# Performance work log

Hardware: AMD Instinct MI355X
Metric: run time of the kernel (lower is better)

The kernel has to match this reference:

```python
import jax, jax.numpy as jnp
import numpy as np

DIM = 4096
N_HEADS = 32
HEAD_DIM = 128
N_KV_HEADS = 8
KV_REPEATS = N_HEADS // N_KV_HEADS
SLIDING_WINDOW = 4096
SEQLEN = 2048
SCALE = HEAD_DIM ** -0.5
NEG = -1e9


def calculate_rope(x, cos, sin):
    # x: [S, H, D]; cos/sin: [S, D//2] applied to interleaved channel pairs
    x1, x2 = x[..., ::2], x[..., 1::2]
    c, s = cos[:, None, :], sin[:, None, :]
    r1 = x1 * c - x2 * s
    r2 = x1 * s + x2 * c
    return jnp.stack([r1, r2], axis=-1).reshape(x.shape)


def setup_inputs() -> dict:
    key = jax.random.key(0)
    ks = jax.random.split(key, 8)
    x = jax.random.normal(ks[0], (SEQLEN, DIM), dtype=jnp.float32)
    # rotary tables
    inv_freq = 1.0 / (10000.0 ** (np.arange(0, HEAD_DIM, 2, dtype=np.float32) / HEAD_DIM))
    t = np.arange(SEQLEN, dtype=np.float32)
    freqs = np.outer(t, inv_freq)  # [S, D/2]
    cos_freq = jnp.asarray(np.cos(freqs), dtype=jnp.float32)
    sin_freq = jnp.asarray(np.sin(freqs), dtype=jnp.float32)
    positions = jnp.arange(SEQLEN, dtype=jnp.int32)
    # causal sliding-window additive mask
    i = np.arange(SEQLEN)[:, None]
    j = np.arange(SEQLEN)[None, :]
    allow = (j <= i) & (j > i - SLIDING_WINDOW)
    mask = jnp.asarray(np.where(allow, 0.0, NEG), dtype=jnp.float32)
    cache_k = jnp.zeros((SLIDING_WINDOW, N_KV_HEADS, HEAD_DIM), dtype=jnp.float32)
    cache_v = jnp.zeros((SLIDING_WINDOW, N_KV_HEADS, HEAD_DIM), dtype=jnp.float32)
    # eqx.nn.Linear weights have shape (out_features, in_features)
    sd = DIM ** -0.5
    wq = jax.random.normal(ks[1], (N_HEADS * HEAD_DIM, DIM), dtype=jnp.float32) * sd
    wk = jax.random.normal(ks[2], (N_KV_HEADS * HEAD_DIM, DIM), dtype=jnp.float32) * sd
    wv = jax.random.normal(ks[3], (N_KV_HEADS * HEAD_DIM, DIM), dtype=jnp.float32) * sd
    wo = jax.random.normal(ks[4], (DIM, N_HEADS * HEAD_DIM), dtype=jnp.float32) * (N_HEADS * HEAD_DIM) ** -0.5
    return {"x": x, "cos_freq": cos_freq, "sin_freq": sin_freq, "positions": positions,
            "mask": mask, "cache_k": cache_k, "cache_v": cache_v,
            "wq": wq, "wk": wk, "wv": wv, "wo": wo}


def reference(x, cos_freq, sin_freq, positions, mask, cache_k, cache_v, wq, wk, wv, wo):
    seqlen = x.shape[0]
    xq = (x @ wq.T).reshape(seqlen, N_HEADS, HEAD_DIM)
    xk = (x @ wk.T).reshape(seqlen, N_KV_HEADS, HEAD_DIM)
    xv = (x @ wv.T).reshape(seqlen, N_KV_HEADS, HEAD_DIM)
    xq = calculate_rope(xq, cos_freq, sin_freq)
    xk = calculate_rope(xk, cos_freq, sin_freq)
    # prefill branch (positions.shape[0] > 1): scatter into sliding-window cache
    cache_k = cache_k.at[positions, :, :].set(xk[positions, :, :], mode='drop')
    cache_v = cache_v.at[positions, :, :].set(xv[positions, :, :], mode='drop')
    # GQA repeat kv heads
    k = jnp.repeat(xk, KV_REPEATS, axis=1)  # [S, H, D]
    v = jnp.repeat(xv, KV_REPEATS, axis=1)
    # scores: [H, Sq, Sk]
    scores = jnp.einsum('qhd,khd->hqk', xq, k) * SCALE
    scores = scores + mask[None, ...]
    probs = jax.nn.softmax(scores.astype(jnp.float32), axis=-1).astype(xq.dtype)
    out = jnp.einsum('hqk,khd->qhd', probs, v).reshape(seqlen, N_HEADS * HEAD_DIM)
    output = out @ wo.T
    return output, cache_k, cache_v
```

## Files before the change

### kernel.cpp

```cpp
#include <hip/hip_runtime.h>

typedef unsigned short ushort_t;
typedef unsigned int uint_t;
typedef __attribute__((ext_vector_type(8))) short bf16x8;
typedef __attribute__((ext_vector_type(4))) float floatx4;
typedef __attribute__((ext_vector_type(16))) float floatx16;

#define SEQ 2048
#define DIM 4096
#define NH 32
#define NKV 8
#define HD 128
#define KVDIM 1024
#define QKVN 6144

__device__ __forceinline__ ushort_t f2b(float f) {
  union { float f; uint_t u; } x; x.f = f;
  uint_t u = x.u;
  u += 0x7fffu + ((u >> 16) & 1u);
  return (ushort_t)(u >> 16);
}

#define GLOAD_LDS(g, l) \
  __builtin_amdgcn_global_load_lds((const __attribute__((address_space(1))) void*)(g), \
                                   (__attribute__((address_space(3))) void*)(l), 16, 0, 0)

#define BARX() asm volatile("s_barrier" ::: "memory")
#define WAIT_VM(n) asm volatile("s_waitcnt vmcnt(" #n ")" ::: "memory")

__global__ __launch_bounds__(256) void cvt_all(const float* __restrict__ x,
                                               const float* __restrict__ wq,
                                               const float* __restrict__ wk,
                                               const float* __restrict__ wv,
                                               const float* __restrict__ wo,
                                               ushort_t* __restrict__ xb,
                                               ushort_t* __restrict__ wqkvb,
                                               ushort_t* __restrict__ wob) {
  int b = blockIdx.x;
  const float* src; ushort_t* dst; int i;
  if (b < 4096)       { src = x;  dst = xb;               i = b * 256 + threadIdx.x; }
  else if (b < 12288) { src = wq; dst = wqkvb;            i = (b - 4096) * 256 + threadIdx.x; }
  else if (b < 14336) { src = wk; dst = wqkvb + 16777216; i = (b - 12288) * 256 + threadIdx.x; }
  else if (b < 16384) { src = wv; dst = wqkvb + 20971520; i = (b - 14336) * 256 + threadIdx.x; }
  else                { src = wo; dst = wob;              i = (b - 16384) * 256 + threadIdx.x; }
  const float4* s = (const float4*)src;
  float4 a = s[2 * i], c = s[2 * i + 1];
  union { ushort_t u[8]; uint4 v; } o;
  o.u[0] = f2b(a.x); o.u[1] = f2b(a.y); o.u[2] = f2b(a.z); o.u[3] = f2b(a.w);
  o.u[4] = f2b(c.x); o.u[5] = f2b(c.y); o.u[6] = f2b(c.z); o.u[7] = f2b(c.w);
  ((uint4*)dst)[i] = o.v;
}

__global__ __launch_bounds__(512, 2) void gemm8p(const ushort_t* __restrict__ A,
                                                 const ushort_t* __restrict__ B,
                                                 float* __restrict__ C,
                                                 int N, int K) {
  __shared__ __attribute__((aligned(16))) ushort_t sA[2][8192];
  __shared__ __attribute__((aligned(16))) ushort_t sB[2][16384];

  int tid = threadIdx.x;
  int lane = tid & 63;
  int w = tid >> 6;
  int wm = w >> 2, wn = w & 3;
  int l15 = lane & 15, l4 = lane >> 4;
  int e7 = l15 & 7;
  int co0 = ((l4 ^ e7) << 3);
  int co1 = co0 ^ 32;

  int nwg = (int)gridDim.x;
  int ntn = N >> 8;
  int lin = ((int)blockIdx.x & 7) * (nwg >> 3) + ((int)blockIdx.x >> 3);
  int m0 = (lin / ntn) << 7;
  int n0 = (lin % ntn) << 8;

  int nkt = K >> 6;
  int niter = nkt >> 1;

  int r0 = tid >> 3;
  int c0 = ((tid & 7) ^ (r0 & 7)) << 3;
  const ushort_t* sa0 = A + (size_t)(m0 + r0) * K + c0;
  const ushort_t* sb0 = B + (size_t)(n0 + r0) * K + c0;
  const ushort_t* sb1 = sb0 + (size_t)128 * K;
  int d0 = (tid & ~63) << 3;
  size_t ek = (size_t)64 * K;

#define STA(kk, s)  do { GLOAD_LDS(sa0 + (kk), &sA[s][d0]); \
                         GLOAD_LDS(sa0 + ek + (kk), &sA[s][d0 + 4096]); } while (0)
#define STB0(kk, s) do { GLOAD_LDS(sb0 + (kk), &sB[s][d0]); \
                         GLOAD_LDS(sb0 + ek + (kk), &sB[s][d0 + 4096]); } while (0)
#define STB1(kk, s) do { GLOAD_LDS(sb1 + (kk), &sB[s][8192 + d0]); \
                         GLOAD_LDS(sb1 + ek + (kk), &sB[s][8192 + d0 + 4096]); } while (0)

  floatx4 acc[4][4] = {};
  bf16x8 a[4][2], b[4][2];

#define RDA2(s, RG) do { const ushort_t* pa = &sA[s][(wm * 64 + l15) * 64]; \
  _Pragma("unroll") for (int rg = 0; rg < 2; ++rg) { \
    a[RG + rg][0] = *(const bf16x8*)&pa[(RG + rg) * 1024 + co0]; \
    a[RG + rg][1] = *(const bf16x8*)&pa[(RG + rg) * 1024 + co1]; } } while (0)
#define RDB2(s, CG) do { const ushort_t* pb = &sB[s][(wn * 64 + l15) * 64]; \
  _Pragma("unroll") for (int cg = 0; cg < 2; ++cg) { \
    b[CG + cg][0] = *(const bf16x8*)&pb[(CG + cg) * 1024 + co0]; \
    b[CG + cg][1] = *(const bf16x8*)&pb[(CG + cg) * 1024 + co1]; } } while (0)

#define QUAD(RG, CG) do { __builtin_amdgcn_s_setprio(1); \
  _Pragma("unroll") for (int rg = 0; rg < 2; ++rg) \
  _Pragma("unroll") for (int cg = 0; cg < 2; ++cg) \
  _Pragma("unroll") for (int ks = 0; ks < 2; ++ks) \
    acc[RG + rg][CG + cg] = __builtin_amdgcn_mfma_f32_16x16x32_bf16( \
        a[RG + rg][ks], b[CG + cg][ks], acc[RG + rg][CG + cg], 0, 0, 0); \
  __builtin_amdgcn_s_setprio(0); } while (0)

  STA(0, 0); STB0(0, 0); STB1(0, 0);
  STA(64, 1); STB0(64, 1);
  WAIT_VM(4);
  BARX();

#pragma unroll 1
  for (int i = 0; i < niter; ++i) {
    int k1 = (2 * i + 1) << 6;
    int t2 = 2 * i + 2; if (t2 > nkt - 1) t2 = nkt - 1;
    int t3 = 2 * i + 3; if (t3 > nkt - 1) t3 = nkt - 1;
    int k2 = t2 << 6, k3 = t3 << 6;

    RDA2(0, 0); RDB2(0, 0); RDA2(0, 2);
    STB1(k1, 1);
    BARX(); QUAD(0, 0); BARX();
    RDB2(0, 2);
    STA(k2, 0);
    BARX(); QUAD(0, 2); BARX();
    STB0(k2, 0);
    BARX(); QUAD(2, 0); BARX();
    STB1(k2, 0);
    WAIT_VM(6);
    BARX(); QUAD(2, 2); BARX();

    RDA2(1, 0); RDB2(1, 0); RDA2(1, 2);
    BARX(); QUAD(0, 0); BARX();
    RDB2(1, 2);
    STA(k3, 1);
    BARX(); QUAD(0, 2); BARX();
    STB0(k3, 1);
    BARX(); QUAD(2, 0); BARX();
    WAIT_VM(4);
    BARX(); QUAD(2, 2); BARX();
  }

#pragma unroll
  for (int rg = 0; rg < 4; ++rg)
#pragma unroll
    for (int cg = 0; cg < 4; ++cg) {
      float* cp = C + (size_t)(m0 + wm * 64 + rg * 16 + l4 * 4) * N
                    + (n0 + wn * 64 + cg * 16 + l15);
#pragma unroll
      for (int r = 0; r < 4; ++r) cp[(size_t)r * N] = acc[rg][cg][r];
    }
#undef STA
#undef STB0
#undef STB1
#undef RDA2
#undef RDB2
#undef QUAD
}

__global__ __launch_bounds__(256) void posteps(const float* __restrict__ qkv,
                                               const float* __restrict__ cosf,
                                               const float* __restrict__ sinf,
                                               ushort_t* __restrict__ qb,
                                               ushort_t* __restrict__ kb,
                                               float* __restrict__ out) {
  int b = blockIdx.x;
  if (b < 16384) {
    const float QS = 1.4426950408889634f * 0.08838834764831845f;
    int idx = b * 256 + threadIdx.x;
    int pos = idx >> 11;
    int p = idx & 2047;
    int h = p >> 6, i = p & 63;
    size_t sb = (size_t)pos * QKVN + h * HD + 2 * i;
    float x1 = qkv[sb], x2 = qkv[sb + 1];
    float c = cosf[pos * 64 + i], s = sinf[pos * 64 + i];
    float r1 = (x1 * c - x2 * s) * QS;
    float r2 = (x1 * s + x2 * c) * QS;
    size_t db = (size_t)pos * DIM + h * HD + 2 * i;
    ((uint_t*)qb)[db >> 1] = (uint_t)f2b(r1) | ((uint_t)f2b(r2) << 16);
  } else if (b < 20480) {
    int idx = (b - 16384) * 256 + threadIdx.x;
    int pos = idx >> 9;
    int p = idx & 511;
    int kvh = p >> 6, i = p & 63;
    size_t sb = (size_t)pos * QKVN + DIM + kvh * HD + 2 * i;
    float x1 = qkv[sb], x2 = qkv[sb + 1];
    float c = cosf[pos * 64 + i], s = sinf[pos * 64 + i];
    float r1 = x1 * c - x2 * s;
    float r2 = x1 * s + x2 * c;
    size_t db = (size_t)pos * KVDIM + kvh * HD + 2 * i;
    ((uint_t*)kb)[db >> 1] = (uint_t)f2b(r1) | ((uint_t)f2b(r2) << 16);
    float2 cv; cv.x = r1; cv.y = r2;
    ((float2*)(out + 8388608))[db >> 1] = cv;
  } else {
    int i = (b - 20480) * 256 + threadIdx.x;
    float4 z = {0.f, 0.f, 0.f, 0.f};
    ((float4*)(out + 10485760))[i] = z;
    ((float4*)(out + 14680064))[i] = z;
  }
}

__global__ __launch_bounds__(256) void vt_cache(const float* __restrict__ qkv,
                                                ushort_t* __restrict__ vtb,
                                                float* __restrict__ cache_v) {
  __shared__ float tile[64][65];
  int pos0 = blockIdx.x * 64, c0 = blockIdx.y * 64;
  int t = threadIdx.x;
  int pr = t >> 4, cq = (t & 15) * 4;
#pragma unroll
  for (int rr = 0; rr < 4; ++rr) {
    int prow = pr + rr * 16;
    float4 v = *(const float4*)(qkv + (size_t)(pos0 + prow) * QKVN + DIM + KVDIM + c0 + cq);
    *(float4*)(cache_v + (size_t)(pos0 + prow) * KVDIM + c0 + cq) = v;
    tile[prow][cq] = v.x; tile[prow][cq + 1] = v.y;
    tile[prow][cq + 2] = v.z; tile[prow][cq + 3] = v.w;
  }
  __syncthreads();
  int dc = t >> 2, pg = (t & 3) * 16;
  int kvh = c0 >> 7, dl = (c0 & 127) + dc;
  union { ushort_t u[16]; uint4 q[2]; } o;
#pragma unroll
  for (int e = 0; e < 16; ++e) o.u[e] = f2b(tile[pg + e][dc]);
  uint4* dst = (uint4*)(vtb + (size_t)kvh * (HD * SEQ) + (size_t)dl * SEQ + pos0 + pg);
  dst[0] = o.q[0]; dst[1] = o.q[1];
}

__global__ __launch_bounds__(256) void attn(const ushort_t* __restrict__ Q,
                                            const ushort_t* __restrict__ Kb,
                                            const ushort_t* __restrict__ Vt,
                                            ushort_t* __restrict__ O) {
  int h = blockIdx.y;
  int kvh = h >> 2;
  int tid = threadIdx.x;
  int w = tid >> 6, lane = tid & 63;
  int row = lane & 15, quad = lane >> 4;

  __shared__ __attribute__((aligned(16))) ushort_t lds_k[64][136];
  __shared__ __attribute__((aligned(16))) ushort_t lds_vt[128][72];
  __shared__ __attribute__((aligned(16))) float p_lds[4][16][68];

  int kr = tid >> 2, kc = (tid & 3) * 32;
  int vd = tid >> 1, vj = (tid & 1) * 32;
  const ushort_t* kg = Kb + (size_t)kr * KVDIM + kvh * HD + kc;
  const ushort_t* vg = Vt + (size_t)kvh * (HD * SEQ) + (size_t)vd * SEQ + vj;

#pragma unroll 1
  for (int ph = 0; ph < 2; ++ph) {
    int qb = ph ? (31 - blockIdx.x) : blockIdx.x;
    int q0 = qb * 64 + w * 16;

    bf16x8 qf[4];
    const ushort_t* qp = Q + (size_t)(q0 + row) * DIM + h * HD + quad * 8;
#pragma unroll
    for (int ks = 0; ks < 4; ++ks) qf[ks] = *(const bf16x8*)(qp + ks * 32);

    floatx4 o_acc[8] = {};
    float l_r[4] = {0.f, 0.f, 0.f, 0.f};

    for (int kt = 0; kt <= qb; ++kt) {
      int kv0 = kt * 64;
#pragma unroll
      for (int e = 0; e < 4; ++e)
        *(bf16x8*)&lds_k[kr][kc + e * 8] = *(const bf16x8*)(kg + (size_t)kv0 * KVDIM + e * 8);
#pragma unroll
      for (int e = 0; e < 4; ++e)
        *(bf16x8*)&lds_vt[vd][vj + e * 8] = *(const bf16x8*)(vg + kv0 + e * 8);
      __syncthreads();

      floatx4 s[4] = {};
#pragma unroll
      for (int j2 = 0; j2 < 4; ++j2)
#pragma unroll
        for (int ks = 0; ks < 4; ++ks) {
          bf16x8 kfrag = *(const bf16x8*)&lds_k[j2 * 16 + row][ks * 32 + quad * 8];
          s[j2] = __builtin_amdgcn_mfma_f32_16x16x32_bf16(qf[ks], kfrag, s[j2], 0, 0, 0);
        }

      bool diag = (kt == qb);
      float pv[4][4];
#pragma unroll
      for (int j2 = 0; j2 < 4; ++j2)
#pragma unroll
        for (int r = 0; r < 4; ++r) {
          float v = s[j2][r];
          if (diag) {
            int j_g = kv0 + j2 * 16 + row;
            int i_g = q0 + quad * 4 + r;
            v += (j_g <= i_g) ? 0.f : -1e9f;
          }
          float p = exp2f(v);
          pv[j2][r] = p;
          l_r[r] += p;
        }
#pragma unroll
      for (int j2 = 0; j2 < 4; ++j2)
#pragma unroll
        for (int r = 0; r < 4; ++r) p_lds[w][quad * 4 + r][j2 * 16 + row] = pv[j2][r];
      bf16x8 pf[2];
#pragma unroll
      for (int kb2 = 0; kb2 < 2; ++kb2) {
        float4 pa = *(const float4*)&p_lds[w][row][kb2 * 32 + quad * 8];
        float4 pb = *(const float4*)&p_lds[w][row][kb2 * 32 + quad * 8 + 4];
        union { bf16x8 v; ushort_t u[8]; } pu;
        pu.u[0] = f2b(pa.x); pu.u[1] = f2b(pa.y); pu.u[2] = f2b(pa.z); pu.u[3] = f2b(pa.w);
        pu.u[4] = f2b(pb.x); pu.u[5] = f2b(pb.y); pu.u[6] = f2b(pb.z); pu.u[7] = f2b(pb.w);
        pf[kb2] = pu.v;
      }
#pragma unroll
      for (int db = 0; db < 8; ++db)
#pragma unroll
        for (int kb2 = 0; kb2 < 2; ++kb2) {
          bf16x8 vfrag = *(const bf16x8*)&lds_vt[db * 16 + row][kb2 * 32 + quad * 8];
          o_acc[db] = __builtin_amdgcn_mfma_f32_16x16x32_bf16(pf[kb2], vfrag, o_acc[db], 0, 0, 0);
        }
      __syncthreads();
    }

#pragma unroll
    for (int off = 1; off < 16; off <<= 1)
#pragma unroll
      for (int r = 0; r < 4; ++r) l_r[r] += __shfl_xor(l_r[r], off, 64);
    float inv[4];
#pragma unroll
    for (int r = 0; r < 4; ++r) inv[r] = 1.0f / l_r[r];
#pragma unroll
    for (int db = 0; db < 8; ++db)
#pragma unroll
      for (int r = 0; r < 4; ++r)
        O[(size_t)(q0 + quad * 4 + r) * DIM + h * HD + db * 16 + row] = f2b(o_acc[db][r] * inv[r]);
  }
}

extern "C" void kernel_launch(void* const* d_in, const int* in_sizes, int n_in,
                              void* d_out, int out_size, void* d_ws, size_t ws_size,
                              hipStream_t stream) {
  const float* x    = (const float*)d_in[0];
  const float* cosf = (const float*)d_in[1];
  const float* sinf = (const float*)d_in[2];
  const float* wq = (const float*)d_in[7];
  const float* wk = (const float*)d_in[8];
  const float* wv = (const float*)d_in[9];
  const float* wo = (const float*)d_in[10];
  float* out = (float*)d_out;
  float* cache_v_out = out + 12582912;

  char* ws = (char*)d_ws;
  ushort_t* xb     = (ushort_t*)(ws + 0);
  ushort_t* wqkvb  = (ushort_t*)(ws + 16777216);
  ushort_t* wob    = (ushort_t*)(ws + 67108864);
  float*    qkv32  = (float*)(ws + 100663296);
  ushort_t* qbuf   = (ushort_t*)(ws + 150994944);
  ushort_t* kbuf   = (ushort_t*)(ws + 167772160);
  ushort_t* vtb    = (ushort_t*)(ws + 171966464);
  ushort_t* attnb  = (ushort_t*)(ws + 176160768);

  cvt_all<<<24576, 256, 0, stream>>>(x, wq, wk, wv, wo, xb, wqkvb, wob);
  gemm8p<<<384, 512, 0, stream>>>(xb, wqkvb, qkv32, QKVN, DIM);
  posteps<<<22528, 256, 0, stream>>>(qkv32, cosf, sinf, qbuf, kbuf, out);
  vt_cache<<<dim3(32, 16), 256, 0, stream>>>(qkv32, vtb, cache_v_out);
  attn<<<dim3(16, 32), 256, 0, stream>>>(qbuf, kbuf, vtb, attnb);
  gemm8p<<<256, 512, 0, stream>>>(attnb, wob, out, DIM, DIM);
}
```

Baseline: 594.6 us.

## Transpose GEMM block tile to 256x128 and simplify the pipelined k-loop schedule

Both GEMMs now use a 256(M) x 128(N) block tile instead of 128x256, with waves laid out 4x2 instead of 2x4. Block-to-tile mapping is hard-coded to M=2048, which holds for both launches. Each k-tile is now split into two MFMA phases instead of four, with explicit lgkmcnt waits and fewer barriers, aiming to cut synchronisation overhead and improve overlap of global-to-LDS loads with compute. The LDS footprint and per-wave register use are unchanged, but the new load and wait ordering may expose more latency.

```diff
diff --git a/kernel.cpp b/kernel.cpp
--- a/kernel.cpp
+++ b/kernel.cpp
@@ -4,7 +4,6 @@
 typedef unsigned int uint_t;
 typedef __attribute__((ext_vector_type(8))) short bf16x8;
 typedef __attribute__((ext_vector_type(4))) float floatx4;
-typedef __attribute__((ext_vector_type(16))) float floatx16;
 
 #define SEQ 2048
 #define DIM 4096
@@ -27,6 +26,7 @@
 
 #define BARX() asm volatile("s_barrier" ::: "memory")
 #define WAIT_VM(n) asm volatile("s_waitcnt vmcnt(" #n ")" ::: "memory")
+#define LGKM0() asm volatile("s_waitcnt lgkmcnt(0)" ::: "memory")
 
 __global__ __launch_bounds__(256) void cvt_all(const float* __restrict__ x,
                                                const float* __restrict__ wq,
@@ -51,99 +51,98 @@
   ((uint4*)dst)[i] = o.v;
 }
 
-__global__ __launch_bounds__(512, 2) void gemm8p(const ushort_t* __restrict__ A,
+__global__ __launch_bounds__(512, 2) void gemm2p(const ushort_t* __restrict__ A,
                                                  const ushort_t* __restrict__ B,
                                                  float* __restrict__ C,
                                                  int N, int K) {
-  __shared__ __attribute__((aligned(16))) ushort_t sA[2][8192];
-  __shared__ __attribute__((aligned(16))) ushort_t sB[2][16384];
+  __shared__ __attribute__((aligned(16))) ushort_t sA[2][16384];
+  __shared__ __attribute__((aligned(16))) ushort_t sB[2][8192];
 
   int tid = threadIdx.x;
   int lane = tid & 63;
   int w = tid >> 6;
-  int wm = w >> 2, wn = w & 3;
+  int wm = w >> 1, wn = w & 1;
   int l15 = lane & 15, l4 = lane >> 4;
-  int e7 = l15 & 7;
-  int co0 = ((l4 ^ e7) << 3);
+  int co0 = (l4 ^ (l15 & 7)) << 3;
   int co1 = co0 ^ 32;
 
-  int nwg = (int)gridDim.x;
-  int ntn = N >> 8;
-  int lin = ((int)blockIdx.x & 7) * (nwg >> 3) + ((int)blockIdx.x >> 3);
-  int m0 = (lin / ntn) << 7;
-  int n0 = (lin % ntn) << 8;
+  int nblk = (int)gridDim.x;
+  int lin = ((int)blockIdx.x & 7) * (nblk >> 3) + ((int)blockIdx.x >> 3);
+  int m0 = (lin & 7) << 8;
+  int n0 = (lin >> 3) << 7;
 
   int nkt = K >> 6;
   int niter = nkt >> 1;
 
   int r0 = tid >> 3;
-  int c0 = ((tid & 7) ^ (r0 & 7)) << 3;
-  const ushort_t* sa0 = A + (size_t)(m0 + r0) * K + c0;
-  const ushort_t* sb0 = B + (size_t)(n0 + r0) * K + c0;
-  const ushort_t* sb1 = sb0 + (size_t)128 * K;
-  int d0 = (tid & ~63) << 3;
-  size_t ek = (size_t)64 * K;
-
-#define STA(kk, s)  do { GLOAD_LDS(sa0 + (kk), &sA[s][d0]); \
-                         GLOAD_LDS(sa0 + ek + (kk), &sA[s][d0 + 4096]); } while (0)
-#define STB0(kk, s) do { GLOAD_LDS(sb0 + (kk), &sB[s][d0]); \
-                         GLOAD_LDS(sb0 + ek + (kk), &sB[s][d0 + 4096]); } while (0)
-#define STB1(kk, s) do { GLOAD_LDS(sb1 + (kk), &sB[s][8192 + d0]); \
-                         GLOAD_LDS(sb1 + ek + (kk), &sB[s][8192 + d0 + 4096]); } while (0)
+  int cg8 = ((tid & 7) ^ (r0 & 7)) << 3;
+  const ushort_t* sa = A + (size_t)(m0 + r0) * K + cg8;
+  const ushort_t* sb = B + (size_t)(n0 + r0) * K + cg8;
+  int ldsb = (tid & ~63) << 3;
+  size_t rK = (size_t)64 * K;
+
+#define SUA(s, uu, k0) GLOAD_LDS(sa + (size_t)(uu) * rK + (k0), &sA[s][(uu) * 4096 + ldsb])
+#define SUB(s, uu, k0) GLOAD_LDS(sb + (size_t)(uu) * rK + (k0), &sB[s][(uu) * 4096 + ldsb])
 
   floatx4 acc[4][4] = {};
   bf16x8 a[4][2], b[4][2];
 
-#define RDA2(s, RG) do { const ushort_t* pa = &sA[s][(wm * 64 + l15) * 64]; \
-  _Pragma("unroll") for (int rg = 0; rg < 2; ++rg) { \
-    a[RG + rg][0] = *(const bf16x8*)&pa[(RG + rg) * 1024 + co0]; \
-    a[RG + rg][1] = *(const bf16x8*)&pa[(RG + rg) * 1024 + co1]; } } while (0)
-#define RDB2(s, CG) do { const ushort_t* pb = &sB[s][(wn * 64 + l15) * 64]; \
+#define RDA(s) do { const ushort_t* pa = &sA[s][(wm * 64 + l15) * 64]; \
+  _Pragma("unroll") for (int rg = 0; rg < 4; ++rg) { \
+    a[rg][0] = *(const bf16x8*)&pa[rg * 1024 + co0]; \
+    a[rg][1] = *(const bf16x8*)&pa[rg * 1024 + co1]; } } while (0)
+#define RDB01(s) do { const ushort_t* pb = &sB[s][(wn * 64 + l15) * 64]; \
   _Pragma("unroll") for (int cg = 0; cg < 2; ++cg) { \
-    b[CG + cg][0] = *(const bf16x8*)&pb[(CG + cg) * 1024 + co0]; \
-    b[CG + cg][1] = *(const bf16x8*)&pb[(CG + cg) * 1024 + co1]; } } while (0)
-
-#define QUAD(RG, CG) do { __builtin_amdgcn_s_setprio(1); \
-  _Pragma("unroll") for (int rg = 0; rg < 2; ++rg) \
-  _Pragma("unroll") for (int cg = 0; cg < 2; ++cg) \
+    b[cg][0] = *(const bf16x8*)&pb[cg * 1024 + co0]; \
+    b[cg][1] = *(const bf16x8*)&pb[cg * 1024 + co1]; } } while (0)
+#define RDB23(s) do { const ushort_t* pb = &sB[s][(wn * 64 + l15) * 64]; \
+  _Pragma("unroll") for (int cg = 2; cg < 4; ++cg) { \
+    b[cg][0] = *(const bf16x8*)&pb[cg * 1024 + co0]; \
+    b[cg][1] = *(const bf16x8*)&pb[cg * 1024 + co1]; } } while (0)
+
+#define QUAD(CG) do { __builtin_amdgcn_s_setprio(1); \
+  _Pragma("unroll") for (int rg = 0; rg < 4; ++rg) \
+  _Pragma("unroll") for (int cg = CG; cg < CG + 2; ++cg) \
   _Pragma("unroll") for (int ks = 0; ks < 2; ++ks) \
-    acc[RG + rg][CG + cg] = __builtin_amdgcn_mfma_f32_16x16x32_bf16( \
-        a[RG + rg][ks], b[CG + cg][ks], acc[RG + rg][CG + cg], 0, 0, 0); \
+    acc[rg][cg] = __builtin_amdgcn_mfma_f32_16x16x32_bf16( \
+        a[rg][ks], b[cg][ks], acc[rg][cg], 0, 0, 0); \
   __builtin_amdgcn_s_setprio(0); } while (0)
 
-  STA(0, 0); STB0(0, 0); STB1(0, 0);
-  STA(64, 1); STB0(64, 1);
+  SUA(0, 0, 0); SUA(0, 1, 0); SUA(0, 2, 0); SUA(0, 3, 0);
+  SUB(0, 0, 0); SUB(0, 1, 0);
+  SUA(1, 0, 64); SUA(1, 1, 64); SUA(1, 2, 64); SUA(1, 3, 64);
   WAIT_VM(4);
   BARX();
 
 #pragma unroll 1
   for (int i = 0; i < niter; ++i) {
-    int k1 = (2 * i + 1) << 6;
-    int t2 = 2 * i + 2; if (t2 > nkt - 1) t2 = nkt - 1;
-    int t3 = 2 * i + 3; if (t3 > nkt - 1) t3 = nkt - 1;
-    int k2 = t2 << 6, k3 = t3 << 6;
-
-    RDA2(0, 0); RDB2(0, 0); RDA2(0, 2);
-    STB1(k1, 1);
-    BARX(); QUAD(0, 0); BARX();
-    RDB2(0, 2);
-    STA(k2, 0);
-    BARX(); QUAD(0, 2); BARX();
-    STB0(k2, 0);
-    BARX(); QUAD(2, 0); BARX();
-    STB1(k2, 0);
-    WAIT_VM(6);
-    BARX(); QUAD(2, 2); BARX();
-
-    RDA2(1, 0); RDB2(1, 0); RDA2(1, 2);
-    BARX(); QUAD(0, 0); BARX();
-    RDB2(1, 2);
-    STA(k3, 1);
-    BARX(); QUAD(0, 2); BARX();
-    STB0(k3, 1);
-    BARX(); QUAD(2, 0); BARX();
+    int kv = (2 * i + 1) << 6;
+    int tu2 = 2 * i + 2; if (tu2 > nkt - 1) tu2 = nkt - 1;
+    int tv2 = 2 * i + 3; if (tv2 > nkt - 1) tv2 = nkt - 1;
+    int ku2 = tu2 << 6, kv2 = tv2 << 6;
+
+    RDA(0); RDB01(0);
+    SUB(1, 0, kv); SUB(1, 1, kv);
+    BARX(); LGKM0();
+    QUAD(0);
+    BARX();
+    RDB23(0);
+    SUA(0, 0, ku2); SUA(0, 1, ku2); SUA(0, 2, ku2); SUA(0, 3, ku2);
+    BARX(); LGKM0();
+    QUAD(2);
     WAIT_VM(4);
-    BARX(); QUAD(2, 2); BARX();
+    BARX();
+    RDA(1); RDB01(1);
+    SUB(0, 0, ku2); SUB(0, 1, ku2);
+    BARX(); LGKM0();
+    QUAD(0);
+    BARX();
+    RDB23(1);
+    SUA(1, 0, kv2); SUA(1, 1, kv2); SUA(1, 2, kv2); SUA(1, 3, kv2);
+    BARX(); LGKM0();
+    QUAD(2);
+    WAIT_VM(4);
+    BARX();
   }
 
 #pragma unroll
@@ -155,11 +154,11 @@
 #pragma unroll
       for (int r = 0; r < 4; ++r) cp[(size_t)r * N] = acc[rg][cg][r];
     }
-#undef STA
-#undef STB0
-#undef STB1
-#undef RDA2
-#undef RDB2
+#undef SUA
+#undef SUB
+#undef RDA
+#undef RDB01
+#undef RDB23
 #undef QUAD
 }
 
@@ -360,9 +359,9 @@
   ushort_t* attnb  = (ushort_t*)(ws + 176160768);
 
   cvt_all<<<24576, 256, 0, stream>>>(x, wq, wk, wv, wo, xb, wqkvb, wob);
-  gemm8p<<<384, 512, 0, stream>>>(xb, wqkvb, qkv32, QKVN, DIM);
+  gemm2p<<<384, 512, 0, stream>>>(xb, wqkvb, qkv32, QKVN, DIM);
   posteps<<<22528, 256, 0, stream>>>(qkv32, cosf, sinf, qbuf, kbuf, out);
   vt_cache<<<dim3(32, 16), 256, 0, stream>>>(qkv32, vtb, cache_v_out);
   attn<<<dim3(16, 32), 256, 0, stream>>>(qbuf, kbuf, vtb, attnb);
-  gemm8p<<<256, 512, 0, stream>>>(attnb, wob, out, DIM, DIM);
-}
+  gemm2p<<<256, 512, 0, stream>>>(attnb, wob, out, DIM, DIM);
+}
```

After: 597.7 us. Within noise of the previous version (+0.5%).
